# Performance work log

Measured on AMD Instinct MI355X. Metric: run time of the kernel, lower is better.

The kernel has to match this reference:

```python
import jax, jax.numpy as jnp
import numpy as np


def setup_inputs() -> dict:
    key = jax.random.key(0)
    k1, k2 = jax.random.split(key)
    x = jax.random.normal(k1, (16, 1, 512, 512), dtype=jnp.float32)
    weight = jax.random.normal(k2, (128, 1), dtype=jnp.float32)
    return {"x": x, "weight": weight}


def reference(x, weight):
    # x: [B, C=1, H, W]; weight: [K=128, D=1] codebook
    inputs = jnp.transpose(x, (0, 2, 3, 1))          # [B, H, W, C]
    input_shape = inputs.shape
    D = weight.shape[1]
    flat = inputs.reshape(-1, D)                     # [N, D]
    # pairwise squared distances: ||z||^2 + ||e||^2 - 2 z.e^T  -> [N, K]
    dist = (jnp.sum(flat ** 2, axis=1, keepdims=True)
            + jnp.sum(weight ** 2, axis=1)
            - 2.0 * flat @ weight.T)
    idx = jnp.argmin(dist, axis=1)                   # [N]
    # one-hot @ weight == gather of codebook rows (same math, no [N,K] one-hot)
    quantized = weight[idx].reshape(input_shape)     # [B, H, W, C]
    return jnp.transpose(quantized, (0, 3, 1, 2))    # [B, C, H, W]
```

## Files before the change

kernel.cpp:

```cpp
#include <hip/hip_runtime.h>


constexpr int K     = 128;
constexpr int EPT   = 8;
constexpr int BLOCK = 256;

__global__ __launch_bounds__(BLOCK) void vq_kernel(const float* __restrict__ x,
                                                   const float* __restrict__ w,
                                                   float* __restrict__ out,
                                                   long n, int kk) {
#pragma clang fp contract(off)
    __shared__ float wraw[K];
    __shared__ float sv[K];
    __shared__ int   si[K];
    __shared__ float t8[8];
    __shared__ float t4[16];
    __shared__ float t2[32];
    __shared__ float t1[64];

    const int t = threadIdx.x;
    if (t < K) {
        wraw[t] = (t < kk) ? w[t] : __builtin_inff();
        sv[t]   = __builtin_inff();
        si[t]   = 0x7fffffff;
    }
    __syncthreads();
    if (t < kk) {
        float v = wraw[t];
        int rank = 0;
        for (int j = 0; j < kk; ++j) {
            float u = wraw[j];
            rank += (u < v) || (u == v && j < t);
        }
        sv[rank] = v;
        si[rank] = t;
    }
    __syncthreads();
    if (t < 64) t1[t] = sv[2 * t];
    if (t < 32) t2[t] = sv[4 * t + 1];
    if (t < 16) t4[t] = sv[8 * t + 3];
    if (t < 8)  t8[t] = sv[16 * t + 7];
    __syncthreads();

    const float m1  = sv[63];
    const float m2a = sv[31],  m2b = sv[95];
    const float m3a = sv[15],  m3b = sv[47], m3c = sv[79], m3d = sv[111];
    const int smax = (kk > 8 ? kk : 8) - 8;

    long base = ((long)blockIdx.x * BLOCK + t) * (long)EPT;
    if (base + EPT <= n) {
        float4 a = *(const float4*)(x + base);
        float4 b = *(const float4*)(x + base + 4);
        float xs[EPT] = {a.x, a.y, a.z, a.w, b.x, b.y, b.z, b.w};
        float res[EPT];
#pragma unroll
        for (int e = 0; e < EPT; ++e) {
            float xv = xs[e];
            float x2 = xv * xv;
            asm volatile("" : "+v"(x2));
            float tx = xv + xv;

            int pos = (m1 < xv) ? 64 : 0;
            float m2 = (pos & 64) ? m2b : m2a;
            pos += (m2 < xv) ? 32 : 0;
            float m3lo = (pos & 32) ? m3b : m3a;
            float m3hi = (pos & 32) ? m3d : m3c;
            float m3   = (pos & 64) ? m3hi : m3lo;
            pos += (m3 < xv) ? 16 : 0;
            pos += (t8[pos >> 4] < xv) ? 8 : 0;
            pos += (t4[pos >> 3] < xv) ? 4 : 0;
            pos += (t2[pos >> 2] < xv) ? 2 : 0;
            pos += (t1[pos >> 1] < xv) ? 1 : 0;

            int s = pos - 4;
            s = s < 0 ? 0 : (s > smax ? smax : s);

            float best = __builtin_inff();
            float bw   = 0.0f;
            unsigned tie = 0u;
#pragma unroll
            for (int c = 0; c < 8; ++c) {
                float wv = sv[s + c];
                float w2 = wv * wv;
                asm volatile("" : "+v"(w2));
                float sum  = x2 + w2;
                float prod = tx * wv;
                asm volatile("" : "+v"(prod));
                float d = sum - prod;
                bool lt = d < best;
                tie |= (d == best) ? 1u : 0u;
                best = lt ? d : best;
                bw   = lt ? wv : bw;
            }
            res[e] = bw;
            if (__builtin_expect(tie != 0u, 0)) {
                float bb = __builtin_inff(), bwv = 0.0f;
                int bi = 0x7fffffff;
                for (int c = 0; c < 8; ++c) {
                    float wv = sv[s + c];
                    float w2 = wv * wv;
                    asm volatile("" : "+v"(w2));
                    float sum  = x2 + w2;
                    float prod = tx * wv;
                    asm volatile("" : "+v"(prod));
                    float d = sum - prod;
                    int oi = si[s + c];
                    if (d < bb || (d == bb && oi < bi)) { bb = d; bi = oi; bwv = wv; }
                }
                res[e] = bwv;
            }
        }
        *(float4*)(out + base)     = make_float4(res[0], res[1], res[2], res[3]);
        *(float4*)(out + base + 4) = make_float4(res[4], res[5], res[6], res[7]);
    } else {
        for (long i = base; i < n; ++i) {
            float xv = x[i];
            float x2 = xv * xv;
            asm volatile("" : "+v"(x2));
            float tx = xv + xv;
            float bb = __builtin_inff(), bwv = 0.0f;
            int bi = 0x7fffffff;
            for (int p0 = 0; p0 < kk; ++p0) {
                float wv = sv[p0];
                float w2 = wv * wv;
                asm volatile("" : "+v"(w2));
                float sum  = x2 + w2;
                float prod = tx * wv;
                asm volatile("" : "+v"(prod));
                float d = sum - prod;
                int oi = si[p0];
                if (d < bb || (d == bb && oi < bi)) { bb = d; bi = oi; bwv = wv; }
            }
            out[i] = bwv;
        }
    }
}

extern "C" void kernel_launch(void* const* d_in, const int* in_sizes, int n_in,
                              void* d_out, int out_size, void* d_ws, size_t ws_size,
                              hipStream_t stream) {
    const float* x = (const float*)d_in[0];
    const float* w = (const float*)d_in[1];
    float* out     = (float*)d_out;
    long n = (long)in_sizes[0];
    int  kk = in_sizes[1] < K ? in_sizes[1] : K;

    long threads_needed = (n + EPT - 1) / EPT;
    long grid = (threads_needed + BLOCK - 1) / BLOCK;
    vq_kernel<<<(int)grid, BLOCK, 0, stream>>>(x, w, out, n, kk);
}
```

Measured before the change: 84.87 us.

## Replace per-element binary search with bucketed lookup table over sorted codebook

Each block now builds a 1024-bin lookup table that maps a quantized x value to a candidate window of sorted codebook entries. This replaces the seven-level binary search done per element. Squared codebook values are precomputed once into shared memory instead of being recomputed for every candidate. It also adds a rare extended scan when a bin's window exceeds 8 entries. The cost is a heavier per-block setup phase (1024 bins with binary searches) and more shared memory, and correctness depends on the DELTA margin covering rounding near bin edges.

New measurement: 90.74 us. 1.07x slower.

```diff
diff --git a/kernel.cpp b/kernel.cpp
--- a/kernel.cpp
+++ b/kernel.cpp
@@ -2,8 +2,11 @@
 
 
 constexpr int K     = 128;
+constexpr int NB    = 1024;
 constexpr int EPT   = 8;
 constexpr int BLOCK = 256;
+
+#define DELTA 0.0125f
 
 __global__ __launch_bounds__(BLOCK) void vq_kernel(const float* __restrict__ x,
                                                    const float* __restrict__ w,
@@ -11,18 +14,16 @@
                                                    long n, int kk) {
 #pragma clang fp contract(off)
     __shared__ float wraw[K];
-    __shared__ float sv[K];
+    __shared__ float svw[2 * K];
     __shared__ int   si[K];
-    __shared__ float t8[8];
-    __shared__ float t4[16];
-    __shared__ float t2[32];
-    __shared__ float t1[64];
+    __shared__ int   lut[NB];
 
     const int t = threadIdx.x;
     if (t < K) {
-        wraw[t] = (t < kk) ? w[t] : __builtin_inff();
-        sv[t]   = __builtin_inff();
-        si[t]   = 0x7fffffff;
+        wraw[t]    = (t < kk) ? w[t] : __builtin_inff();
+        svw[t]     = __builtin_inff();
+        svw[K + t] = __builtin_inff();
+        si[t]      = 0x7fffffff;
     }
     __syncthreads();
     if (t < kk) {
@@ -32,26 +33,55 @@
             float u = wraw[j];
             rank += (u < v) || (u == v && j < t);
         }
-        sv[rank] = v;
-        si[rank] = t;
+        float v2 = v * v;
+        asm volatile("" : "+v"(v2));
+        svw[rank]     = v;
+        svw[K + rank] = v2;
+        si[rank]      = t;
     }
     __syncthreads();
-    if (t < 64) t1[t] = sv[2 * t];
-    if (t < 32) t2[t] = sv[4 * t + 1];
-    if (t < 16) t4[t] = sv[8 * t + 3];
-    if (t < 8)  t8[t] = sv[16 * t + 7];
+
+    const float lo    = svw[0];
+    const float hi    = svw[kk - 1];
+    const float range = hi - lo;
+    const float scale = (range > 0.f) ? (float)NB / range : 0.f;
+    const float binv  = (range > 0.f) ? range / (float)NB : 0.f;
+    const int   sMax  = (kk > 8 ? kk : 8) - 8;
+
+    for (int b = t; b < NB; b += BLOCK) {
+        float L = lo + ((float)b - 1.5f) * binv;
+        float R = lo + ((float)b + 2.5f) * binv;
+        int pL = 0;
+#pragma unroll
+        for (int st = 64; st > 0; st >>= 1)
+            if (svw[pL + st - 1] < L) pL += st;
+        if (svw[pL] < L) ++pL;
+        int pR = 0;
+#pragma unroll
+        for (int st = 64; st > 0; st >>= 1)
+            if (svw[pR + st - 1] < R) pR += st;
+        if (svw[pR] < R) ++pR;
+
+        float wa  = svw[pL > 0 ? pL - 1 : 0];
+        float wb  = svw[pR < kk ? pR : kk - 1];
+        float tlo = wa - DELTA;
+        float thi = wb + DELTA;
+
+        int s0 = pL > 0 ? pL - 1 : 0;
+        while (s0 > 0 && svw[s0 - 1] >= tlo) --s0;
+        int e0 = pR;
+        while (e0 < kk && svw[e0] <= thi) ++e0;
+
+        if (s0 > sMax) s0 = sMax;
+        lut[b] = s0 | (e0 << 8);
+    }
     __syncthreads();
-
-    const float m1  = sv[63];
-    const float m2a = sv[31],  m2b = sv[95];
-    const float m3a = sv[15],  m3b = sv[47], m3c = sv[79], m3d = sv[111];
-    const int smax = (kk > 8 ? kk : 8) - 8;
 
     long base = ((long)blockIdx.x * BLOCK + t) * (long)EPT;
     if (base + EPT <= n) {
-        float4 a = *(const float4*)(x + base);
-        float4 b = *(const float4*)(x + base + 4);
-        float xs[EPT] = {a.x, a.y, a.z, a.w, b.x, b.y, b.z, b.w};
+        float4 a  = *(const float4*)(x + base);
+        float4 b4 = *(const float4*)(x + base + 4);
+        float xs[EPT] = {a.x, a.y, a.z, a.w, b4.x, b4.y, b4.z, b4.w};
         float res[EPT];
 #pragma unroll
         for (int e = 0; e < EPT; ++e) {
@@ -60,29 +90,20 @@
             asm volatile("" : "+v"(x2));
             float tx = xv + xv;
 
-            int pos = (m1 < xv) ? 64 : 0;
-            float m2 = (pos & 64) ? m2b : m2a;
-            pos += (m2 < xv) ? 32 : 0;
-            float m3lo = (pos & 32) ? m3b : m3a;
-            float m3hi = (pos & 32) ? m3d : m3c;
-            float m3   = (pos & 64) ? m3hi : m3lo;
-            pos += (m3 < xv) ? 16 : 0;
-            pos += (t8[pos >> 4] < xv) ? 8 : 0;
-            pos += (t4[pos >> 3] < xv) ? 4 : 0;
-            pos += (t2[pos >> 2] < xv) ? 2 : 0;
-            pos += (t1[pos >> 1] < xv) ? 1 : 0;
-
-            int s = pos - 4;
-            s = s < 0 ? 0 : (s > smax ? smax : s);
+            float fi = (xv - lo) * scale;
+            int idx = (int)fi;
+            idx = idx < 0 ? 0 : (idx > NB - 1 ? NB - 1 : idx);
+            int pk = lut[idx];
+            int s  = pk & 0xff;
+            int en = pk >> 8;
 
             float best = __builtin_inff();
             float bw   = 0.0f;
             unsigned tie = 0u;
 #pragma unroll
             for (int c = 0; c < 8; ++c) {
-                float wv = sv[s + c];
-                float w2 = wv * wv;
-                asm volatile("" : "+v"(w2));
+                float wv = svw[s + c];
+                float w2 = svw[K + s + c];
                 float sum  = x2 + w2;
                 float prod = tx * wv;
                 asm volatile("" : "+v"(prod));
@@ -92,19 +113,33 @@
                 best = lt ? d : best;
                 bw   = lt ? wv : bw;
             }
-            res[e] = bw;
-            if (__builtin_expect(tie != 0u, 0)) {
-                float bb = __builtin_inff(), bwv = 0.0f;
-                int bi = 0x7fffffff;
-                for (int c = 0; c < 8; ++c) {
-                    float wv = sv[s + c];
-                    float w2 = wv * wv;
-                    asm volatile("" : "+v"(w2));
+            if (__builtin_expect(en > s + 8, 0)) {
+                for (int j = s + 8; j < en; ++j) {
+                    float wv = svw[j];
+                    float w2 = svw[K + j];
                     float sum  = x2 + w2;
                     float prod = tx * wv;
                     asm volatile("" : "+v"(prod));
                     float d = sum - prod;
-                    int oi = si[s + c];
+                    bool lt = d < best;
+                    tie |= (d == best) ? 1u : 0u;
+                    best = lt ? d : best;
+                    bw   = lt ? wv : bw;
+                }
+            }
+            res[e] = bw;
+            if (__builtin_expect(tie != 0u, 0)) {
+                int hiEnd = en > s + 8 ? en : s + 8;
+                float bb = __builtin_inff(), bwv = 0.0f;
+                int bi = 0x7fffffff;
+                for (int j = s; j < hiEnd; ++j) {
+                    float wv = svw[j];
+                    float w2 = svw[K + j];
+                    float sum  = x2 + w2;
+                    float prod = tx * wv;
+                    asm volatile("" : "+v"(prod));
+                    float d = sum - prod;
+                    int oi = si[j];
                     if (d < bb || (d == bb && oi < bi)) { bb = d; bi = oi; bwv = wv; }
                 }
                 res[e] = bwv;
@@ -121,9 +156,8 @@
             float bb = __builtin_inff(), bwv = 0.0f;
             int bi = 0x7fffffff;
             for (int p0 = 0; p0 < kk; ++p0) {
-                float wv = sv[p0];
-                float w2 = wv * wv;
-                asm volatile("" : "+v"(w2));
+                float wv = svw[p0];
+                float w2 = svw[K + p0];
                 float sum  = x2 + w2;
                 float prod = tx * wv;
                 asm volatile("" : "+v"(prod));
```
